# Kernel tuning notes

Measured on AMD Instinct MI355X. Metric: run time of the kernel, lower is better.

The kernel has to match this reference:

```python
import jax, jax.numpy as jnp
import numpy as np

EPS = 1e-05
KEEP_RATIO = 0.7


def setup_inputs() -> dict:
    key = jax.random.key(0)
    ks = jax.random.split(key, 10)
    B, C, L, H = 8, 512, 8192, 128
    return {
        "x": jax.random.normal(ks[0], (B, C, L), dtype=jnp.float32),
        "c": jax.random.normal(ks[1], (B, C, L), dtype=jnp.float32),
        "gw1": jax.random.normal(ks[2], (H, C), dtype=jnp.float32) * 0.05,
        "gb1": jax.random.normal(ks[3], (H,), dtype=jnp.float32) * 0.05,
        "gw2": jax.random.normal(ks[4], (C, H), dtype=jnp.float32) * 0.05,
        "gb2": jax.random.normal(ks[5], (C,), dtype=jnp.float32) * 0.05,
        "mw1": jax.random.normal(ks[6], (H, C), dtype=jnp.float32) * 0.05,
        "mb1": jax.random.normal(ks[7], (H,), dtype=jnp.float32) * 0.05,
        "mw2": jax.random.normal(ks[8], (2 * C, H), dtype=jnp.float32) * 0.05,
        "mb2": jax.random.normal(ks[9], (2 * C,), dtype=jnp.float32) * 0.05,
    }


def reference(x, c, gw1, gb1, gw2, gb2, mw1, mb1, mw2, mb2):
    B, C, L = x.shape
    # per-channel stats over L
    mu_c = jnp.mean(x, axis=2, keepdims=True)                 # [B,C,1]
    var_c = jnp.var(x, axis=2, keepdims=True)                 # ddof=0
    sigma_c = jnp.sqrt(var_c + EPS)
    # per-sample stats over (C,L)
    mu_l = jnp.mean(x, axis=(1, 2), keepdims=True)            # [B,1,1]
    var_l = jnp.var(x, axis=(1, 2), keepdims=True)
    sigma_l = jnp.sqrt(var_l + EPS)
    # gate network on c (1x1 convs == channel matmuls), then mean over L
    h = jax.nn.relu(jnp.einsum('hc,bcl->bhl', gw1, c) + gb1[None, :, None])
    g = jax.nn.sigmoid(jnp.einsum('ch,bhl->bcl', gw2, h) + gb2[None, :, None])
    g_mix = jnp.mean(g, axis=2, keepdims=True)                # [B,C,1]
    mu = g_mix * mu_c + (1.0 - g_mix) * mu_l
    sigma = g_mix * sigma_c + (1.0 - g_mix) * sigma_l
    x_hat = (x - mu) / sigma
    # MLP on pooled condition -> gamma, beta
    cond_pool = jnp.mean(c, axis=2)                           # [B,C]
    hm = jax.nn.relu(jnp.einsum('hc,bc->bh', mw1, cond_pool) + mb1)
    gamma_beta = jnp.einsum('oh,bh->bo', mw2, hm) + mb2       # [B,2C]
    gamma = gamma_beta[:, :C][:, :, None]                     # [B,C,1]
    beta = gamma_beta[:, C:][:, :, None]
    y = (1.0 + gamma) * x_hat + beta
    # top-k channel mask by mean |y| over L
    imp = jnp.mean(jnp.abs(y), axis=2)                        # [B,C]
    k = max(1, int(C * KEEP_RATIO))
    _, idx = jax.lax.top_k(imp, k)                            # [B,k]
    mask = jnp.zeros((B, C), dtype=y.dtype).at[jnp.arange(B)[:, None], idx].set(1.0)
    return y * mask[:, :, None]
```

## Files before the change

### kernel.cpp

```cpp
#include <hip/hip_runtime.h>
#include <hip/hip_bf16.h>
#include <math.h>

#define NB 8
#define NC 512
#define NL 8192
#define NH 128
#define FEPS 1e-5f
#define NKEEP 358

typedef __attribute__((ext_vector_type(8))) short short8;
typedef __attribute__((ext_vector_type(4))) float f32x4;

__device__ __forceinline__ unsigned short f2bf(float x) {
  unsigned u = __float_as_uint(x);
  return (unsigned short)((u + 0x7fffu + ((u >> 16) & 1u)) >> 16);
}
__device__ __forceinline__ unsigned pack2(float a, float b) {
  return (unsigned)f2bf(a) | ((unsigned)f2bf(b) << 16);
}

__global__ __launch_bounds__(256) void k0_prep(
    const float* __restrict__ gw1, const float* __restrict__ gw2,
    unsigned short* __restrict__ gw1b, unsigned short* __restrict__ gw2b,
    float* __restrict__ csum, float* __restrict__ gsum) {
  int i = blockIdx.x * 256 + threadIdx.x;
  gw1b[i] = f2bf(gw1[i]);
  gw2b[i] = f2bf(gw2[i]);
  if (i < NB * NC) { csum[i] = 0.f; gsum[i] = 0.f; }
}

__global__ __launch_bounds__(256) void k1_xstats(
    const float* __restrict__ x, float* __restrict__ xsum, float* __restrict__ xsumsq) {
  int bc = blockIdx.x;
  int t = threadIdx.x;
  const float4* xp = reinterpret_cast<const float4*>(x + (size_t)bc * NL);
  float s1 = 0.f, s2 = 0.f;
#pragma unroll
  for (int i = 0; i < 8; ++i) {
    float4 v = xp[i * 256 + t];
    s1 += v.x + v.y + v.z + v.w;
    s2 += v.x * v.x + v.y * v.y + v.z * v.z + v.w * v.w;
  }
  for (int off = 32; off; off >>= 1) { s1 += __shfl_down(s1, off); s2 += __shfl_down(s2, off); }
  __shared__ float r1[4], r2[4];
  if ((t & 63) == 0) { r1[t >> 6] = s1; r2[t >> 6] = s2; }
  __syncthreads();
  if (t == 0) {
    xsum[bc]   = r1[0] + r1[1] + r1[2] + r1[3];
    xsumsq[bc] = r2[0] + r2[1] + r2[2] + r2[3];
  }
}

__global__ __launch_bounds__(256, 2) void k2_gate(
    const float* __restrict__ cin,
    const unsigned short* __restrict__ gw1b, const unsigned short* __restrict__ gw2b,
    const float* __restrict__ gb1, const float* __restrict__ gb2,
    float* __restrict__ gsum_g, float* __restrict__ csum_g) {
  __shared__ unsigned AsU[128 * 36];
  __shared__ __align__(16) unsigned short Bs[8192];
  __shared__ __align__(16) unsigned short Hts[4][32][136];
  __shared__ float gsum_s[NC], csum_s[NC], gb2_s[NC];
  __shared__ float gb1_s[NH];

  const int t = threadIdx.x;
  const int lane = t & 63;
  const int w = t >> 6;
  const int r = lane & 15;
  const int kg = lane >> 4;
  const int b = blockIdx.x >> 6;
  const int l0 = (blockIdx.x & 63) * 128;

  for (int i = t; i < NC; i += 256) { gsum_s[i] = 0.f; csum_s[i] = 0.f; gb2_s[i] = gb2[i]; }
  if (t < NH) gb1_s[t] = gb1[t];

  const int p  = t >> 3;
  const int q  = t & 7;
  const int brow = lane >> 3;
  const int bs1  = lane & 7;
  const int crow = lane >> 4;
  const int bs2  = lane & 15;

  f32x4 acc0[8], acc1[8];
#pragma unroll
  for (int i = 0; i < 8; ++i) { acc0[i] = (f32x4){0.f,0.f,0.f,0.f}; acc1[i] = (f32x4){0.f,0.f,0.f,0.f}; }

  const float* cbase = cin + (size_t)b * NC * NL + l0;

  for (int k = 0; k < 8; ++k) {
    __syncthreads();
    short8 bv[4];
#pragma unroll
    for (int j = 0; j < 4; ++j) {
      const int h = 32 * w + 8 * j + brow;
      bv[j] = *reinterpret_cast<const short8*>(gw1b + (size_t)h * NC + k * 64 + bs1 * 8);
    }
    float4 va[4], vb[4];
#pragma unroll
    for (int pass = 0; pass < 4; ++pass) {
      const float* cp0 = cbase + (size_t)(k * 64 + 2 * p) * NL + 32 * pass + 4 * q;
      va[pass] = *reinterpret_cast<const float4*>(cp0);
      vb[pass] = *reinterpret_cast<const float4*>(cp0 + NL);
    }
#pragma unroll
    for (int j = 0; j < 4; ++j) {
      const int h = 32 * w + 8 * j + brow;
      *reinterpret_cast<short8*>(&Bs[h * 64 + ((bs1 ^ brow) * 8)]) = bv[j];
    }
    float sa = 0.f, sb = 0.f;
#pragma unroll
    for (int pass = 0; pass < 4; ++pass) {
      const int ll = 32 * pass + 4 * q;
      sa += va[pass].x + va[pass].y + va[pass].z + va[pass].w;
      sb += vb[pass].x + vb[pass].y + vb[pass].z + vb[pass].w;
      AsU[(ll + 0) * 36 + p] = pack2(va[pass].x, vb[pass].x);
      AsU[(ll + 1) * 36 + p] = pack2(va[pass].y, vb[pass].y);
      AsU[(ll + 2) * 36 + p] = pack2(va[pass].z, vb[pass].z);
      AsU[(ll + 3) * 36 + p] = pack2(va[pass].w, vb[pass].w);
    }
    sa += __shfl_xor(sa, 1); sa += __shfl_xor(sa, 2); sa += __shfl_xor(sa, 4);
    sb += __shfl_xor(sb, 1); sb += __shfl_xor(sb, 2); sb += __shfl_xor(sb, 4);
    if ((lane & 7) == 0) {
      atomicAdd(&csum_s[k * 64 + 2 * p],     sa);
      atomicAdd(&csum_s[k * 64 + 2 * p + 1], sb);
    }
    __syncthreads();
#pragma unroll
    for (int kk = 0; kk < 2; ++kk) {
      const short8 a0 = *reinterpret_cast<const short8*>(&AsU[(32 * w + r)      * 36 + 16 * kk + 4 * kg]);
      const short8 a1 = *reinterpret_cast<const short8*>(&AsU[(32 * w + 16 + r) * 36 + 16 * kk + 4 * kg]);
#pragma unroll
      for (int ht = 0; ht < 8; ++ht) {
        const short8 bf = *reinterpret_cast<const short8*>(
            &Bs[(16 * ht + r) * 64 + (((4 * kk + kg) ^ (r & 7)) * 8)]);
        acc0[ht] = __builtin_amdgcn_mfma_f32_16x16x32_bf16(a0, bf, acc0[ht], 0, 0, 0);
        acc1[ht] = __builtin_amdgcn_mfma_f32_16x16x32_bf16(a1, bf, acc1[ht], 0, 0, 0);
      }
    }
  }

#pragma unroll
  for (int ht = 0; ht < 8; ++ht) {
#pragma unroll
    for (int reg = 0; reg < 4; ++reg) {
      const float bias = gb1_s[16 * ht + r];
      Hts[w][4 * kg + reg][16 * ht + r]      = f2bf(fmaxf(acc0[ht][reg] + bias, 0.f));
      Hts[w][16 + 4 * kg + reg][16 * ht + r] = f2bf(fmaxf(acc1[ht][reg] + bias, 0.f));
    }
  }
  short8 af0[4], af1[4];
#pragma unroll
  for (int kk = 0; kk < 4; ++kk) {
    af0[kk] = *reinterpret_cast<const short8*>(&Hts[w][r][32 * kk + 8 * kg]);
    af1[kk] = *reinterpret_cast<const short8*>(&Hts[w][16 + r][32 * kk + 8 * kg]);
  }

  for (int cc = 0; cc < 8; ++cc) {
    __syncthreads();
    short8 bv[4];
#pragma unroll
    for (int j = 0; j < 4; ++j) {
      const int cl = 16 * w + 4 * j + crow;
      bv[j] = *reinterpret_cast<const short8*>(gw2b + (size_t)(cc * 64 + cl) * NH + bs2 * 8);
    }
#pragma unroll
    for (int j = 0; j < 4; ++j) {
      const int cl = 16 * w + 4 * j + crow;
      *reinterpret_cast<short8*>(&Bs[cl * 128 + ((bs2 ^ (cl & 7)) * 8)]) = bv[j];
    }
    __syncthreads();
#pragma unroll
    for (int ctt = 0; ctt < 4; ++ctt) {
      f32x4 z0 = (f32x4){0.f,0.f,0.f,0.f}, z1 = (f32x4){0.f,0.f,0.f,0.f};
#pragma unroll
      for (int kk = 0; kk < 4; ++kk) {
        const short8 bf = *reinterpret_cast<const short8*>(
            &Bs[(16 * ctt + r) * 128 + (((4 * kk + kg) ^ (r & 7)) * 8)]);
        z0 = __builtin_amdgcn_mfma_f32_16x16x32_bf16(af0[kk], bf, z0, 0, 0, 0);
        z1 = __builtin_amdgcn_mfma_f32_16x16x32_bf16(af1[kk], bf, z1, 0, 0, 0);
      }
      const float bias = gb2_s[cc * 64 + 16 * ctt + r];
      float s = 0.f;
#pragma unroll
      for (int reg = 0; reg < 4; ++reg) {
        s += 1.f / (1.f + __expf(-(z0[reg] + bias)));
        s += 1.f / (1.f + __expf(-(z1[reg] + bias)));
      }
      s += __shfl_xor(s, 16);
      s += __shfl_xor(s, 32);
      if (lane < 16) atomicAdd(&gsum_s[cc * 64 + 16 * ctt + lane], s);
    }
  }
  __syncthreads();
  for (int i = t; i < NC; i += 256) {
    atomicAdd(&gsum_g[b * NC + i], gsum_s[i]);
    atomicAdd(&csum_g[b * NC + i], csum_s[i]);
  }
}

__global__ __launch_bounds__(256) void k3_final(
    const float* __restrict__ xsum, const float* __restrict__ xsumsq,
    const float* __restrict__ csum, const float* __restrict__ gsum,
    const float* __restrict__ mw1, const float* __restrict__ mb1,
    const float* __restrict__ mw2, const float* __restrict__ mb2,
    float* __restrict__ a_arr, float* __restrict__ d_arr) {
  __shared__ __align__(16) float cp[NC];
  __shared__ __align__(16) float hm[NH];
  __shared__ float gbv[2 * NC];
  __shared__ double red[8];
  __shared__ float mu_l_s, sig_l_s;
  const int b = blockIdx.x, t = threadIdx.x;

  double s1 = 0.0, s2 = 0.0;
  for (int c = t; c < NC; c += 256) { s1 += (double)xsum[b * NC + c]; s2 += (double)xsumsq[b * NC + c]; }
  for (int off = 32; off; off >>= 1) { s1 += __shfl_down(s1, off); s2 += __shfl_down(s2, off); }
  if ((t & 63) == 0) { red[(t >> 6) * 2] = s1; red[(t >> 6) * 2 + 1] = s2; }
  for (int c = t; c < NC; c += 256) cp[c] = csum[b * NC + c] * (1.f / NL);
  __syncthreads();
  if (t == 0) {
    double S1 = red[0] + red[2] + red[4] + red[6];
    double S2 = red[1] + red[3] + red[5] + red[7];
    double n = (double)NC * NL;
    double mu = S1 / n;
    double var = S2 / n - mu * mu;
    mu_l_s = (float)mu;
    sig_l_s = (float)sqrt(var + (double)FEPS);
  }
  __syncthreads();
  if (t < NH) {
    const float4* row = reinterpret_cast<const float4*>(mw1 + (size_t)t * NC);
    const float4* cpv = reinterpret_cast<const float4*>(cp);
    float acc = mb1[t];
    for (int i = 0; i < NC / 4; ++i) {
      float4 wv = row[i], xv = cpv[i];
      acc += wv.x * xv.x + wv.y * xv.y + wv.z * xv.z + wv.w * xv.w;
    }
    hm[t] = fmaxf(acc, 0.f);
  }
  __syncthreads();
  for (int o = t; o < 2 * NC; o += 256) {
    const float4* row = reinterpret_cast<const float4*>(mw2 + (size_t)o * NH);
    const float4* hv = reinterpret_cast<const float4*>(hm);
    float acc = mb2[o];
    for (int i = 0; i < NH / 4; ++i) {
      float4 wv = row[i], xv = hv[i];
      acc += wv.x * xv.x + wv.y * xv.y + wv.z * xv.z + wv.w * xv.w;
    }
    gbv[o] = acc;
  }
  __syncthreads();
  const float mu_l = mu_l_s, sig_l = sig_l_s;
  for (int c = t; c < NC; c += 256) {
    float gm = gsum[b * NC + c] * (1.f / NL);
    double mu_c = (double)xsum[b * NC + c] / NL;
    double var_c = (double)xsumsq[b * NC + c] / NL - mu_c * mu_c;
    float sig_c = (float)sqrt(var_c + (double)FEPS);
    float mu = gm * (float)mu_c + (1.f - gm) * mu_l;
    float sg = gm * sig_c + (1.f - gm) * sig_l;
    float gamma = gbv[c], beta = gbv[NC + c];
    float A = (1.f + gamma) / sg;
    a_arr[b * NC + c] = A;
    d_arr[b * NC + c] = beta - A * mu;
  }
}

__global__ __launch_bounds__(256) void k4_y(
    const float* __restrict__ x, const float* __restrict__ a_arr,
    const float* __restrict__ d_arr, float* __restrict__ out, float* __restrict__ imp) {
  const int bc = blockIdx.x, t = threadIdx.x;
  const float A = a_arr[bc], D = d_arr[bc];
  const float4* xp = reinterpret_cast<const float4*>(x + (size_t)bc * NL);
  float4* op = reinterpret_cast<float4*>(out + (size_t)bc * NL);
  float s = 0.f;
#pragma unroll
  for (int i = 0; i < 8; ++i) {
    float4 v = xp[i * 256 + t];
    float4 y;
    y.x = fmaf(A, v.x, D); y.y = fmaf(A, v.y, D);
    y.z = fmaf(A, v.z, D); y.w = fmaf(A, v.w, D);
    s += fabsf(y.x) + fabsf(y.y) + fabsf(y.z) + fabsf(y.w);
    op[i * 256 + t] = y;
  }
  for (int off = 32; off; off >>= 1) s += __shfl_down(s, off);
  __shared__ float rs[4];
  if ((t & 63) == 0) rs[t >> 6] = s;
  __syncthreads();
  if (t == 0) imp[bc] = rs[0] + rs[1] + rs[2] + rs[3];
}

__global__ __launch_bounds__(512) void k5_mask(
    const float* __restrict__ imp, float* __restrict__ mask) {
  __shared__ float v[NC];
  const int b = blockIdx.x, t = threadIdx.x;
  v[t] = imp[b * NC + t];
  __syncthreads();
  const float mine = v[t];
  int rank = 0;
  for (int j = 0; j < NC; ++j) {
    float o = v[j];
    rank += (o > mine) || (o == mine && j < t);
  }
  mask[b * NC + t] = (rank < NKEEP) ? 1.f : 0.f;
}

__global__ __launch_bounds__(256) void k6_apply(
    const float* __restrict__ mask, float* __restrict__ out) {
  const int bc = blockIdx.x;
  if (mask[bc] != 0.f) return;
  float4* op = reinterpret_cast<float4*>(out + (size_t)bc * NL);
  const float4 z = {0.f, 0.f, 0.f, 0.f};
#pragma unroll
  for (int i = 0; i < 8; ++i) op[i * 256 + threadIdx.x] = z;
}

extern "C" void kernel_launch(void* const* d_in, const int* in_sizes, int n_in,
                              void* d_out, int out_size, void* d_ws, size_t ws_size,
                              hipStream_t stream) {
  const float* x   = (const float*)d_in[0];
  const float* c   = (const float*)d_in[1];
  const float* gw1 = (const float*)d_in[2];
  const float* gb1 = (const float*)d_in[3];
  const float* gw2 = (const float*)d_in[4];
  const float* gb2 = (const float*)d_in[5];
  const float* mw1 = (const float*)d_in[6];
  const float* mb1 = (const float*)d_in[7];
  const float* mw2 = (const float*)d_in[8];
  const float* mb2 = (const float*)d_in[9];
  float* out = (float*)d_out;
  char* ws = (char*)d_ws;

  unsigned short* gw1b = (unsigned short*)(ws);
  unsigned short* gw2b = (unsigned short*)(ws + 131072);
  float* xsum   = (float*)(ws + 262144);
  float* xsumsq = (float*)(ws + 278528);
  float* csum   = (float*)(ws + 294912);
  float* gsum   = (float*)(ws + 311296);
  float* a_arr  = (float*)(ws + 327680);
  float* d_arr  = (float*)(ws + 344064);
  float* imp    = (float*)(ws + 360448);
  float* mask   = (float*)(ws + 376832);

  k0_prep<<<256, 256, 0, stream>>>(gw1, gw2, gw1b, gw2b, csum, gsum);
  k1_xstats<<<NB * NC, 256, 0, stream>>>(x, xsum, xsumsq);
  k2_gate<<<NB * (NL / 128), 256, 0, stream>>>(c, gw1b, gw2b, gb1, gb2, gsum, csum);
  k3_final<<<NB, 256, 0, stream>>>(xsum, xsumsq, csum, gsum, mw1, mb1, mw2, mb2, a_arr, d_arr);
  k4_y<<<NB * NC, 256, 0, stream>>>(x, a_arr, d_arr, out, imp);
  k5_mask<<<NB, 512, 0, stream>>>(imp, mask);
  k6_apply<<<NB * NC, 256, 0, stream>>>(mask, out);
}
```

Measured before the change: 197.1 us.

## Double-buffer gate GEMM tiles, fuse prep and mask kernels, add nontemporal accesses

The weight conversion is folded into the x-stats kernel, and the rank-based mask is merged with the zeroing kernel, removing two launches. In the gate kernel the c-tile load for the next K chunk now overlaps the current MFMA work through double-buffered shared memory. gw1 fragments are read straight from global memory instead of being staged in LDS, and the second GEMM's weight tiles are double-buffered as well. Streaming loads and stores in the gate and y kernels use nontemporal hints, and the rank count in the mask kernel is recomputed redundantly for every (b,c) block.

```diff
diff --git a/kernel.cpp b/kernel.cpp
--- a/kernel.cpp
+++ b/kernel.cpp
@@ -20,20 +20,19 @@
   return (unsigned)f2bf(a) | ((unsigned)f2bf(b) << 16);
 }
 
-__global__ __launch_bounds__(256) void k0_prep(
+__global__ __launch_bounds__(256) void k1_xstats(
+    const float* __restrict__ x, float* __restrict__ xsum, float* __restrict__ xsumsq,
     const float* __restrict__ gw1, const float* __restrict__ gw2,
     unsigned short* __restrict__ gw1b, unsigned short* __restrict__ gw2b,
     float* __restrict__ csum, float* __restrict__ gsum) {
-  int i = blockIdx.x * 256 + threadIdx.x;
-  gw1b[i] = f2bf(gw1[i]);
-  gw2b[i] = f2bf(gw2[i]);
-  if (i < NB * NC) { csum[i] = 0.f; gsum[i] = 0.f; }
-}
-
-__global__ __launch_bounds__(256) void k1_xstats(
-    const float* __restrict__ x, float* __restrict__ xsum, float* __restrict__ xsumsq) {
-  int bc = blockIdx.x;
-  int t = threadIdx.x;
+  const int bc = blockIdx.x;
+  const int t = threadIdx.x;
+  if (bc < 256) {
+    const int i = bc * 256 + t;
+    gw1b[i] = f2bf(gw1[i]);
+    gw2b[i] = f2bf(gw2[i]);
+    if (i < NB * NC) { csum[i] = 0.f; gsum[i] = 0.f; }
+  }
   const float4* xp = reinterpret_cast<const float4*>(x + (size_t)bc * NL);
   float s1 = 0.f, s2 = 0.f;
 #pragma unroll
@@ -57,8 +56,7 @@
     const unsigned short* __restrict__ gw1b, const unsigned short* __restrict__ gw2b,
     const float* __restrict__ gb1, const float* __restrict__ gb2,
     float* __restrict__ gsum_g, float* __restrict__ csum_g) {
-  __shared__ unsigned AsU[128 * 36];
-  __shared__ __align__(16) unsigned short Bs[8192];
+  __shared__ __align__(16) unsigned AsU[2 * 128 * 36];
   __shared__ __align__(16) unsigned short Hts[4][32][136];
   __shared__ float gsum_s[NC], csum_s[NC], gb2_s[NC];
   __shared__ float gb1_s[NH];
@@ -71,79 +69,78 @@
   const int b = blockIdx.x >> 6;
   const int l0 = (blockIdx.x & 63) * 128;
 
+  const int p = t >> 3;
+  const int q = t & 7;
+
+  f32x4 acc0[8], acc1[8];
+#pragma unroll
+  for (int i = 0; i < 8; ++i) { acc0[i] = (f32x4){0.f,0.f,0.f,0.f}; acc1[i] = (f32x4){0.f,0.f,0.f,0.f}; }
+
+  const float* cbase = cin + (size_t)b * NC * NL + l0;
+  const unsigned short* gw1r = gw1b + (size_t)r * NC + kg * 8;
+
+  f32x4 va[4], vb[4];
+
+#define LOADA(kch) { \
+    _Pragma("unroll") \
+    for (int pass = 0; pass < 4; ++pass) { \
+      const float* cp0 = cbase + (size_t)((kch) * 64 + 2 * p) * NL + 32 * pass + 4 * q; \
+      va[pass] = __builtin_nontemporal_load(reinterpret_cast<const f32x4*>(cp0)); \
+      vb[pass] = __builtin_nontemporal_load(reinterpret_cast<const f32x4*>(cp0 + NL)); \
+    } }
+
+#define WRITEA(kch, bufi) { \
+    unsigned* dst = AsU + (bufi) * (128 * 36); \
+    float sa = 0.f, sb = 0.f; \
+    _Pragma("unroll") \
+    for (int pass = 0; pass < 4; ++pass) { \
+      const int ll = 32 * pass + 4 * q; \
+      sa += va[pass].x + va[pass].y + va[pass].z + va[pass].w; \
+      sb += vb[pass].x + vb[pass].y + vb[pass].z + vb[pass].w; \
+      dst[(ll + 0) * 36 + p] = pack2(va[pass].x, vb[pass].x); \
+      dst[(ll + 1) * 36 + p] = pack2(va[pass].y, vb[pass].y); \
+      dst[(ll + 2) * 36 + p] = pack2(va[pass].z, vb[pass].z); \
+      dst[(ll + 3) * 36 + p] = pack2(va[pass].w, vb[pass].w); \
+    } \
+    sa += __shfl_xor(sa, 1); sa += __shfl_xor(sa, 2); sa += __shfl_xor(sa, 4); \
+    sb += __shfl_xor(sb, 1); sb += __shfl_xor(sb, 2); sb += __shfl_xor(sb, 4); \
+    if ((lane & 7) == 0) { \
+      atomicAdd(&csum_s[(kch) * 64 + 2 * p],     sa); \
+      atomicAdd(&csum_s[(kch) * 64 + 2 * p + 1], sb); \
+    } }
+
+  LOADA(0)
   for (int i = t; i < NC; i += 256) { gsum_s[i] = 0.f; csum_s[i] = 0.f; gb2_s[i] = gb2[i]; }
   if (t < NH) gb1_s[t] = gb1[t];
-
-  const int p  = t >> 3;
-  const int q  = t & 7;
-  const int brow = lane >> 3;
-  const int bs1  = lane & 7;
-  const int crow = lane >> 4;
-  const int bs2  = lane & 15;
-
-  f32x4 acc0[8], acc1[8];
-#pragma unroll
-  for (int i = 0; i < 8; ++i) { acc0[i] = (f32x4){0.f,0.f,0.f,0.f}; acc1[i] = (f32x4){0.f,0.f,0.f,0.f}; }
-
-  const float* cbase = cin + (size_t)b * NC * NL + l0;
+  __syncthreads();
+  WRITEA(0, 0)
+  __syncthreads();
 
   for (int k = 0; k < 8; ++k) {
-    __syncthreads();
-    short8 bv[4];
-#pragma unroll
-    for (int j = 0; j < 4; ++j) {
-      const int h = 32 * w + 8 * j + brow;
-      bv[j] = *reinterpret_cast<const short8*>(gw1b + (size_t)h * NC + k * 64 + bs1 * 8);
-    }
-    float4 va[4], vb[4];
-#pragma unroll
-    for (int pass = 0; pass < 4; ++pass) {
-      const float* cp0 = cbase + (size_t)(k * 64 + 2 * p) * NL + 32 * pass + 4 * q;
-      va[pass] = *reinterpret_cast<const float4*>(cp0);
-      vb[pass] = *reinterpret_cast<const float4*>(cp0 + NL);
-    }
-#pragma unroll
-    for (int j = 0; j < 4; ++j) {
-      const int h = 32 * w + 8 * j + brow;
-      *reinterpret_cast<short8*>(&Bs[h * 64 + ((bs1 ^ brow) * 8)]) = bv[j];
-    }
-    float sa = 0.f, sb = 0.f;
-#pragma unroll
-    for (int pass = 0; pass < 4; ++pass) {
-      const int ll = 32 * pass + 4 * q;
-      sa += va[pass].x + va[pass].y + va[pass].z + va[pass].w;
-      sb += vb[pass].x + vb[pass].y + vb[pass].z + vb[pass].w;
-      AsU[(ll + 0) * 36 + p] = pack2(va[pass].x, vb[pass].x);
-      AsU[(ll + 1) * 36 + p] = pack2(va[pass].y, vb[pass].y);
-      AsU[(ll + 2) * 36 + p] = pack2(va[pass].z, vb[pass].z);
-      AsU[(ll + 3) * 36 + p] = pack2(va[pass].w, vb[pass].w);
-    }
-    sa += __shfl_xor(sa, 1); sa += __shfl_xor(sa, 2); sa += __shfl_xor(sa, 4);
-    sb += __shfl_xor(sb, 1); sb += __shfl_xor(sb, 2); sb += __shfl_xor(sb, 4);
-    if ((lane & 7) == 0) {
-      atomicAdd(&csum_s[k * 64 + 2 * p],     sa);
-      atomicAdd(&csum_s[k * 64 + 2 * p + 1], sb);
-    }
-    __syncthreads();
+    const int cur = k & 1;
+    if (k < 7) LOADA(k + 1)
+    const unsigned* Abuf = AsU + cur * (128 * 36);
 #pragma unroll
     for (int kk = 0; kk < 2; ++kk) {
-      const short8 a0 = *reinterpret_cast<const short8*>(&AsU[(32 * w + r)      * 36 + 16 * kk + 4 * kg]);
-      const short8 a1 = *reinterpret_cast<const short8*>(&AsU[(32 * w + 16 + r) * 36 + 16 * kk + 4 * kg]);
+      const short8 a0 = *reinterpret_cast<const short8*>(&Abuf[(32 * w + r)      * 36 + 16 * kk + 4 * kg]);
+      const short8 a1 = *reinterpret_cast<const short8*>(&Abuf[(32 * w + 16 + r) * 36 + 16 * kk + 4 * kg]);
 #pragma unroll
       for (int ht = 0; ht < 8; ++ht) {
         const short8 bf = *reinterpret_cast<const short8*>(
-            &Bs[(16 * ht + r) * 64 + (((4 * kk + kg) ^ (r & 7)) * 8)]);
+            gw1r + (size_t)(ht * 16) * NC + k * 64 + kk * 32);
         acc0[ht] = __builtin_amdgcn_mfma_f32_16x16x32_bf16(a0, bf, acc0[ht], 0, 0, 0);
         acc1[ht] = __builtin_amdgcn_mfma_f32_16x16x32_bf16(a1, bf, acc1[ht], 0, 0, 0);
       }
     }
+    if (k < 7) WRITEA(k + 1, cur ^ 1)
+    __syncthreads();
   }
 
 #pragma unroll
   for (int ht = 0; ht < 8; ++ht) {
+    const float bias = gb1_s[16 * ht + r];
 #pragma unroll
     for (int reg = 0; reg < 4; ++reg) {
-      const float bias = gb1_s[16 * ht + r];
       Hts[w][4 * kg + reg][16 * ht + r]      = f2bf(fmaxf(acc0[ht][reg] + bias, 0.f));
       Hts[w][16 + 4 * kg + reg][16 * ht + r] = f2bf(fmaxf(acc1[ht][reg] + bias, 0.f));
     }
@@ -155,27 +152,38 @@
     af1[kk] = *reinterpret_cast<const short8*>(&Hts[w][16 + r][32 * kk + 8 * kg]);
   }
 
+  unsigned short* Bs2 = reinterpret_cast<unsigned short*>(AsU);
+  const int crow = lane >> 4;
+  const int bs2  = lane & 15;
+  short8 bv[4];
+
+#define LOADB2(ccn) { \
+    _Pragma("unroll") \
+    for (int j = 0; j < 4; ++j) { \
+      const int cl = 16 * w + 4 * j + crow; \
+      bv[j] = *reinterpret_cast<const short8*>(gw2b + (size_t)((ccn) * 64 + cl) * NH + bs2 * 8); \
+    } }
+#define WRITEB2(ccn) { \
+    unsigned short* dstb = Bs2 + ((ccn) & 1) * 8192; \
+    _Pragma("unroll") \
+    for (int j = 0; j < 4; ++j) { \
+      const int cl = 16 * w + 4 * j + crow; \
+      *reinterpret_cast<short8*>(&dstb[cl * 128 + ((bs2 ^ (cl & 7)) * 8)]) = bv[j]; \
+    } }
+
+  LOADB2(0)
+  WRITEB2(0)
+  __syncthreads();
   for (int cc = 0; cc < 8; ++cc) {
-    __syncthreads();
-    short8 bv[4];
-#pragma unroll
-    for (int j = 0; j < 4; ++j) {
-      const int cl = 16 * w + 4 * j + crow;
-      bv[j] = *reinterpret_cast<const short8*>(gw2b + (size_t)(cc * 64 + cl) * NH + bs2 * 8);
-    }
-#pragma unroll
-    for (int j = 0; j < 4; ++j) {
-      const int cl = 16 * w + 4 * j + crow;
-      *reinterpret_cast<short8*>(&Bs[cl * 128 + ((bs2 ^ (cl & 7)) * 8)]) = bv[j];
-    }
-    __syncthreads();
+    if (cc < 7) LOADB2(cc + 1)
+    const unsigned short* Bbuf = Bs2 + (cc & 1) * 8192;
 #pragma unroll
     for (int ctt = 0; ctt < 4; ++ctt) {
       f32x4 z0 = (f32x4){0.f,0.f,0.f,0.f}, z1 = (f32x4){0.f,0.f,0.f,0.f};
 #pragma unroll
       for (int kk = 0; kk < 4; ++kk) {
         const short8 bf = *reinterpret_cast<const short8*>(
-            &Bs[(16 * ctt + r) * 128 + (((4 * kk + kg) ^ (r & 7)) * 8)]);
+            &Bbuf[(16 * ctt + r) * 128 + (((4 * kk + kg) ^ (r & 7)) * 8)]);
         z0 = __builtin_amdgcn_mfma_f32_16x16x32_bf16(af0[kk], bf, z0, 0, 0, 0);
         z1 = __builtin_amdgcn_mfma_f32_16x16x32_bf16(af1[kk], bf, z1, 0, 0, 0);
       }
@@ -190,8 +198,9 @@
       s += __shfl_xor(s, 32);
       if (lane < 16) atomicAdd(&gsum_s[cc * 64 + 16 * ctt + lane], s);
     }
-  }
-  __syncthreads();
+    if (cc < 7) WRITEB2(cc + 1)
+    __syncthreads();
+  }
   for (int i = t; i < NC; i += 256) {
     atomicAdd(&gsum_g[b * NC + i], gsum_s[i]);
     atomicAdd(&csum_g[b * NC + i], csum_s[i]);
@@ -269,17 +278,17 @@
     const float* __restrict__ d_arr, float* __restrict__ out, float* __restrict__ imp) {
   const int bc = blockIdx.x, t = threadIdx.x;
   const float A = a_arr[bc], D = d_arr[bc];
-  const float4* xp = reinterpret_cast<const float4*>(x + (size_t)bc * NL);
-  float4* op = reinterpret_cast<float4*>(out + (size_t)bc * NL);
+  const f32x4* xp = reinterpret_cast<const f32x4*>(x + (size_t)bc * NL);
+  f32x4* op = reinterpret_cast<f32x4*>(out + (size_t)bc * NL);
   float s = 0.f;
 #pragma unroll
   for (int i = 0; i < 8; ++i) {
-    float4 v = xp[i * 256 + t];
-    float4 y;
+    f32x4 v = __builtin_nontemporal_load(xp + i * 256 + t);
+    f32x4 y;
     y.x = fmaf(A, v.x, D); y.y = fmaf(A, v.y, D);
     y.z = fmaf(A, v.z, D); y.w = fmaf(A, v.w, D);
     s += fabsf(y.x) + fabsf(y.y) + fabsf(y.z) + fabsf(y.w);
-    op[i * 256 + t] = y;
+    __builtin_nontemporal_store(y, op + i * 256 + t);
   }
   for (int off = 32; off; off >>= 1) s += __shfl_down(s, off);
   __shared__ float rs[4];
@@ -288,29 +297,31 @@
   if (t == 0) imp[bc] = rs[0] + rs[1] + rs[2] + rs[3];
 }
 
-__global__ __launch_bounds__(512) void k5_mask(
-    const float* __restrict__ imp, float* __restrict__ mask) {
-  __shared__ float v[NC];
-  const int b = blockIdx.x, t = threadIdx.x;
-  v[t] = imp[b * NC + t];
-  __syncthreads();
-  const float mine = v[t];
-  int rank = 0;
-  for (int j = 0; j < NC; ++j) {
-    float o = v[j];
-    rank += (o > mine) || (o == mine && j < t);
-  }
-  mask[b * NC + t] = (rank < NKEEP) ? 1.f : 0.f;
-}
-
-__global__ __launch_bounds__(256) void k6_apply(
-    const float* __restrict__ mask, float* __restrict__ out) {
+__global__ __launch_bounds__(256) void k5_apply(
+    const float* __restrict__ imp, float* __restrict__ out) {
   const int bc = blockIdx.x;
-  if (mask[bc] != 0.f) return;
-  float4* op = reinterpret_cast<float4*>(out + (size_t)bc * NL);
-  const float4 z = {0.f, 0.f, 0.f, 0.f};
-#pragma unroll
-  for (int i = 0; i < 8; ++i) op[i * 256 + threadIdx.x] = z;
+  const int b = bc >> 9;
+  const int c = bc & (NC - 1);
+  const int t = threadIdx.x;
+  const float* row = imp + b * NC;
+  const float mine = row[c];
+  int cnt = 0;
+#pragma unroll
+  for (int jj = 0; jj < 2; ++jj) {
+    const int j = jj * 256 + t;
+    const float o = row[j];
+    cnt += (o > mine) || (o == mine && j < c);
+  }
+  for (int off = 32; off; off >>= 1) cnt += __shfl_down(cnt, off);
+  __shared__ int rs[4];
+  if ((t & 63) == 0) rs[t >> 6] = cnt;
+  __syncthreads();
+  const int rank = rs[0] + rs[1] + rs[2] + rs[3];
+  if (rank < NKEEP) return;
+  f32x4* op = reinterpret_cast<f32x4*>(out + (size_t)bc * NL);
+  const f32x4 z = (f32x4){0.f, 0.f, 0.f, 0.f};
+#pragma unroll
+  for (int i = 0; i < 8; ++i) __builtin_nontemporal_store(z, op + i * 256 + t);
 }
 
 extern "C" void kernel_launch(void* const* d_in, const int* in_sizes, int n_in,
@@ -338,13 +349,10 @@
   float* a_arr  = (float*)(ws + 327680);
   float* d_arr  = (float*)(ws + 344064);
   float* imp    = (float*)(ws + 360448);
-  float* mask   = (float*)(ws + 376832);
-
-  k0_prep<<<256, 256, 0, stream>>>(gw1, gw2, gw1b, gw2b, csum, gsum);
-  k1_xstats<<<NB * NC, 256, 0, stream>>>(x, xsum, xsumsq);
+
+  k1_xstats<<<NB * NC, 256, 0, stream>>>(x, xsum, xsumsq, gw1, gw2, gw1b, gw2b, csum, gsum);
   k2_gate<<<NB * (NL / 128), 256, 0, stream>>>(c, gw1b, gw2b, gb1, gb2, gsum, csum);
   k3_final<<<NB, 256, 0, stream>>>(xsum, xsumsq, csum, gsum, mw1, mb1, mw2, mb2, a_arr, d_arr);
   k4_y<<<NB * NC, 256, 0, stream>>>(x, a_arr, d_arr, out, imp);
-  k5_mask<<<NB, 512, 0, stream>>>(imp, mask);
-  k6_apply<<<NB * NC, 256, 0, stream>>>(mask, out);
-}
+  k5_apply<<<NB * NC, 256, 0, stream>>>(imp, out);
+}
```

Result: faster. 175.9 us (-10.8%).
